# Performance work log

Hardware: AMD Instinct MI355X
Metric: run time of the kernel (lower is better)

The kernel has to match this reference:

```python
import jax, jax.numpy as jnp
import numpy as np

B, S, H, I, G = 2, 1024, 1024, 4096, 8


def setup_inputs() -> dict:
    key = jax.random.key(0)
    k1, k2, k3, k4 = jax.random.split(key, 4)
    # kaiming-style scaled init (scale matters only for numerics, not math)
    hidden_states = jax.random.normal(k1, (B, S, H), dtype=jnp.float32)
    WG = jax.random.normal(k2, (H, G), dtype=jnp.float32) * (1.0 / np.sqrt(H))
    Wi = jax.random.normal(k3, (G, H, I), dtype=jnp.float32) * (1.0 / np.sqrt(H))
    down = jax.random.normal(k4, (I, H), dtype=jnp.float32) * (1.0 / np.sqrt(I))
    return {"hidden_states": hidden_states, "WG": WG, "Wi": Wi, "down": down, "topk": 2}


def topk_sigmoid(gate, k):
    # gate: [B,S,G] -> sigmoid gated scores masked to top-k per token
    _, idx = jax.lax.top_k(gate, k)                       # idx: [B,S,k]
    mask = (idx[..., None] == jnp.arange(gate.shape[-1])).any(axis=-2)  # [B,S,G] bool
    return jax.nn.sigmoid(gate) * mask


def reference(hidden_states, WG, Wi, down, topk):
    gate = hidden_states @ WG                             # [B,S,G]
    g = topk_sigmoid(gate, topk)                          # [B,S,G]
    # dense contraction over all groups (faithful to original einsum)
    up = jnp.einsum('bse,bsg,geo->bso', hidden_states, g, Wi)  # [B,S,I]
    act = jnp.square(jax.nn.relu(up))                     # ReLU^2
    return act @ down                                     # [B,S,H]
```

## Files before the change

kernel.cpp:

```cpp
#include <hip/hip_runtime.h>
#include <hip/hip_bf16.h>

typedef unsigned short u16;
typedef short short8_t __attribute__((ext_vector_type(8)));
typedef float f32x4 __attribute__((ext_vector_type(4)));

#define GLOBAL_AS(p) ((const __attribute__((address_space(1))) void*)(p))
#define LDS_AS(p)    ((__attribute__((address_space(3))) void*)(p))

__device__ __forceinline__ u16 f2bf(float f) {
    union { float f; unsigned int u; } x;
    x.f = f;
    unsigned int r = x.u + 0x7fffu + ((x.u >> 16) & 1u);
    return (u16)(r >> 16);
}

#define M_NMT   0
#define M_TE    2
#define M_TB    42
#define M_PAIR  96
#define M_RTOK  4192
#define M_RW    9312

__global__ __launch_bounds__(64) void gate_topk_kernel(
    const float* __restrict__ h, const float* __restrict__ wg, float* __restrict__ w) {
    const int t = blockIdx.x;
    const int lane = threadIdx.x;
    float acc[8];
#pragma unroll
    for (int g = 0; g < 8; ++g) acc[g] = 0.f;
    for (int e = lane; e < 1024; e += 64) {
        float hv = h[(size_t)t * 1024 + e];
        float4 r0 = *(const float4*)&wg[e * 8];
        float4 r1 = *(const float4*)&wg[e * 8 + 4];
        acc[0] += hv * r0.x; acc[1] += hv * r0.y; acc[2] += hv * r0.z; acc[3] += hv * r0.w;
        acc[4] += hv * r1.x; acc[5] += hv * r1.y; acc[6] += hv * r1.z; acc[7] += hv * r1.w;
    }
#pragma unroll
    for (int off = 32; off > 0; off >>= 1) {
#pragma unroll
        for (int g = 0; g < 8; ++g) acc[g] += __shfl_down(acc[g], off);
    }
    if (lane == 0) {
        int i1 = 0;
        for (int g = 1; g < 8; ++g) if (acc[g] > acc[i1]) i1 = g;
        int i2 = -1;
        for (int g = 0; g < 8; ++g) {
            if (g == i1) continue;
            if (i2 < 0 || acc[g] > acc[i2]) i2 = g;
        }
#pragma unroll
        for (int g = 0; g < 8; ++g) {
            float v = (g == i1 || g == i2) ? (1.f / (1.f + __expf(-acc[g]))) : 0.f;
            w[t * 8 + g] = v;
        }
    }
}

__global__ __launch_bounds__(256) void scan_kernel(
    const float* __restrict__ w, int* __restrict__ meta) {
    __shared__ int cnt[8], pos[8];
    const int tid = threadIdx.x;
    if (tid < 8) cnt[tid] = 0;
    __syncthreads();
    for (int t = tid; t < 2048; t += 256) {
#pragma unroll
        for (int g = 0; g < 8; ++g)
            if (w[t * 8 + g] > 0.f) atomicAdd(&cnt[g], 1);
    }
    __syncthreads();
    if (tid == 0) {
        int base = 0, mt = 0;
        for (int e = 0; e < 8; ++e) {
            pos[e] = base;
            int nt = (cnt[e] + 127) >> 7;
            for (int k = 0; k < nt; ++k) { meta[M_TE + mt] = e; meta[M_TB + mt] = base + k * 128; ++mt; }
            base += nt << 7;
        }
        meta[M_NMT] = mt;
        meta[1] = base;
    }
    __syncthreads();
    for (int i = tid; i < 5120; i += 256) meta[M_RTOK + i] = -1;
    __syncthreads();
    float* row_w = (float*)&meta[M_RW];
    for (int t = tid; t < 2048; t += 256) {
        int slot = 0;
#pragma unroll
        for (int g = 0; g < 8; ++g) {
            float wv = w[t * 8 + g];
            if (wv > 0.f) {
                int p = atomicAdd(&pos[g], 1);
                meta[M_RTOK + p] = t;
                row_w[p] = wv;
                meta[M_PAIR + t * 2 + slot] = p;
                ++slot;
            }
        }
    }
}

__global__ __launch_bounds__(256) void gather_a_kernel(
    const float* __restrict__ h, const int* __restrict__ meta, u16* __restrict__ A) {
    const int row = blockIdx.x;
    const int tid = threadIdx.x;
    const int tok = meta[M_RTOK + row];
    u16* dst = A + (size_t)row * 1024;
    if (tok < 0) {
        uint2 z; z.x = 0u; z.y = 0u;
        ((uint2*)dst)[tid] = z;
        return;
    }
    const float wv = ((const float*)&meta[M_RW])[row];
    float4 v = ((const float4*)(h + (size_t)tok * 1024))[tid];
    u16 o[4] = { f2bf(v.x * wv), f2bf(v.y * wv), f2bf(v.z * wv), f2bf(v.w * wv) };
    ((uint2*)dst)[tid] = *(const uint2*)o;
}

__global__ __launch_bounds__(256, 2) void gemm1_sparse_kernel(
    const u16* __restrict__ A, const float* __restrict__ Wi,
    float* __restrict__ up, const int* __restrict__ meta) {
    const int mt = blockIdx.y;
    if (mt >= meta[M_NMT]) return;
    const int e = meta[M_TE + mt];
    const int base = meta[M_TB + mt];
    const int n0 = blockIdx.x * 128;
    const int K = 1024, N = 4096;
    const float* Bm = Wi + (size_t)e * K * N;

    __shared__ short a_tile[2][128 * 64];
    __shared__ short b_tile[2][128 * 64];
    const int tid = threadIdx.x;
    const int lane = tid & 63;
    const int wave = tid >> 6;
    const int wm = (wave >> 1) * 64;
    const int wn = (wave & 1) * 64;
    const int r = lane & 15;
    const int quad = lane >> 4;
    const int rowin = lane >> 3;
    const int achk = ((lane & 7) ^ (rowin & 7)) * 8;
    const int aldst = (lane & 7) * 8;
    const int bidx_n = tid & 127;
    const int bidx_k8 = tid >> 7;

    const f32x4 vzero = {0.f, 0.f, 0.f, 0.f};
    f32x4 acc[4][4];
#pragma unroll
    for (int i = 0; i < 4; ++i)
#pragma unroll
        for (int j = 0; j < 4; ++j) acc[i][j] = vzero;

    float bvA[4][8], bvB[4][8];

#define G1_LOADB(bv, kb_)                                                             \
    {                                                                                 \
        const int kbc = (kb_);                                                        \
        _Pragma("unroll")                                                             \
        for (int cb = 0; cb < 4; ++cb) {                                              \
            const float* bp = Bm + (size_t)(kbc + (bidx_k8 + cb * 2) * 8) * N + n0 + bidx_n; \
            _Pragma("unroll")                                                         \
            for (int kk = 0; kk < 8; ++kk) bv[cb][kk] = bp[(size_t)kk * N];            \
        }                                                                             \
    }

#define G1_STOREB(bv, buf)                                                            \
    {                                                                                 \
        _Pragma("unroll")                                                             \
        for (int cb = 0; cb < 4; ++cb) {                                              \
            int bk8 = bidx_k8 + cb * 2;                                               \
            u16 bc[8];                                                                \
            _Pragma("unroll")                                                         \
            for (int kk = 0; kk < 8; ++kk) bc[kk] = f2bf(bv[cb][kk]);                  \
            *(short8_t*)&b_tile[buf][bidx_n * 64 + ((bk8 ^ (bidx_n & 7)) * 8)] =       \
                *(const short8_t*)bc;                                                 \
        }                                                                             \
    }

#define G1_STAGEA(kb_, buf)                                                           \
    {                                                                                 \
        const int kbc = (kb_);                                                        \
        _Pragma("unroll")                                                             \
        for (int it = 0; it < 4; ++it) {                                              \
            int row = wave * 8 + it * 32 + rowin;                                     \
            const u16* ga = A + (size_t)(base + row) * K + kbc + achk;                \
            __builtin_amdgcn_global_load_lds(GLOBAL_AS(ga),                           \
                LDS_AS(&a_tile[buf][row * 64 + aldst]), 16, 0, 0);                    \
        }                                                                             \
    }

#define G1_COMPUTE(buf)                                                               \
    {                                                                                 \
        _Pragma("unroll")                                                             \
        for (int ks = 0; ks < 2; ++ks) {                                              \
            const int cp = ((ks * 4 + quad) ^ (r & 7)) * 8;                           \
            short8_t af[4], bfr[4];                                                   \
            _Pragma("unroll")                                                         \
            for (int i = 0; i < 4; ++i)                                               \
                af[i] = *(const short8_t*)&a_tile[buf][(wm + i * 16 + r) * 64 + cp];  \
            _Pragma("unroll")                                                         \
            for (int j = 0; j < 4; ++j)                                               \
                bfr[j] = *(const short8_t*)&b_tile[buf][(wn + j * 16 + r) * 64 + cp]; \
            _Pragma("unroll")                                                         \
            for (int i = 0; i < 4; ++i)                                               \
                _Pragma("unroll")                                                     \
                for (int j = 0; j < 4; ++j)                                           \
                    acc[i][j] = __builtin_amdgcn_mfma_f32_16x16x32_bf16(              \
                        af[i], bfr[j], acc[i][j], 0, 0, 0);                           \
        }                                                                             \
    }

    G1_LOADB(bvA, 0);
    G1_STAGEA(0, 0);
    G1_STOREB(bvA, 0);
    G1_LOADB(bvB, 64);
    __syncthreads();

    for (int t = 0; t < 14; t += 2) {
        G1_LOADB(bvA, (t + 2) * 64);
        __builtin_amdgcn_sched_barrier(0);
        G1_STAGEA((t + 1) * 64, 1);
        G1_STOREB(bvB, 1);
        G1_COMPUTE(0);
        __syncthreads();
        {
            int kbn = (t + 3) * 64; if (kbn > 960) kbn = 960;
            G1_LOADB(bvB, kbn);
        }
        __builtin_amdgcn_sched_barrier(0);
        G1_STAGEA((t + 2) * 64, 0);
        G1_STOREB(bvA, 0);
        G1_COMPUTE(1);
        __syncthreads();
    }
    G1_STAGEA(960, 1);
    G1_STOREB(bvB, 1);
    G1_COMPUTE(0);
    __syncthreads();
    G1_COMPUTE(1);

#undef G1_LOADB
#undef G1_STOREB
#undef G1_STAGEA
#undef G1_COMPUTE

#pragma unroll
    for (int i = 0; i < 4; ++i)
#pragma unroll
        for (int j = 0; j < 4; ++j)
#pragma unroll
            for (int reg = 0; reg < 4; ++reg) {
                int cr = base + wm + i * 16 + quad * 4 + reg;
                int cc = n0 + wn + j * 16 + r;
                up[(size_t)cr * N + cc] = acc[i][j][reg];
            }
}

__global__ __launch_bounds__(256) void combine_kernel(
    const float* __restrict__ up, const int* __restrict__ meta, u16* __restrict__ act) {
    const int t = blockIdx.x;
    const int tid = threadIdx.x;
    const int p0 = meta[M_PAIR + t * 2];
    const int p1 = meta[M_PAIR + t * 2 + 1];
    const float* r0 = up + (size_t)p0 * 4096;
    const float* r1 = up + (size_t)p1 * 4096;
    u16* dst = act + (size_t)t * 4096;
#pragma unroll
    for (int it = 0; it < 4; ++it) {
        int i = (tid + it * 256) * 4;
        float4 a = *(const float4*)&r0[i];
        float4 b = *(const float4*)&r1[i];
        float s0 = a.x + b.x, s1 = a.y + b.y, s2 = a.z + b.z, s3 = a.w + b.w;
        s0 = s0 > 0.f ? s0 * s0 : 0.f;
        s1 = s1 > 0.f ? s1 * s1 : 0.f;
        s2 = s2 > 0.f ? s2 * s2 : 0.f;
        s3 = s3 > 0.f ? s3 * s3 : 0.f;
        u16 o[4] = { f2bf(s0), f2bf(s1), f2bf(s2), f2bf(s3) };
        *(uint2*)&dst[i] = *(const uint2*)o;
    }
}

__global__ __launch_bounds__(256) void transpose_cvt_kernel(
    const float* __restrict__ in, u16* __restrict__ out, int R, int C) {
    __shared__ u16 tile[64][65];
    const int rt = blockIdx.y * 64;
    const int ct = blockIdx.x * 64;
    const int tid = threadIdx.x;
#pragma unroll
    for (int it = 0; it < 2; ++it) {
        int r = (tid >> 3) + it * 32;
        int c8 = (tid & 7) * 8;
        const float* ip = &in[(size_t)(rt + r) * C + ct + c8];
        float4 v0 = *(const float4*)ip;
        float4 v1 = *(const float4*)(ip + 4);
        tile[c8 + 0][r] = f2bf(v0.x); tile[c8 + 1][r] = f2bf(v0.y);
        tile[c8 + 2][r] = f2bf(v0.z); tile[c8 + 3][r] = f2bf(v0.w);
        tile[c8 + 4][r] = f2bf(v1.x); tile[c8 + 5][r] = f2bf(v1.y);
        tile[c8 + 6][r] = f2bf(v1.z); tile[c8 + 7][r] = f2bf(v1.w);
    }
    __syncthreads();
#pragma unroll
    for (int it = 0; it < 2; ++it) {
        int c = (tid >> 3) + it * 32;
        int r8 = (tid & 7) * 8;
        u16 tmp[8];
#pragma unroll
        for (int j = 0; j < 8; ++j) tmp[j] = tile[c][r8 + j];
        *(uint4*)&out[(size_t)(ct + c) * R + rt + r8] = *(const uint4*)tmp;
    }
}

template <int BM, int WROWS, int WCOLS>
__global__ __launch_bounds__(256) void gemm_tn_kernel(
    const u16* __restrict__ X, const u16* __restrict__ Y, float* __restrict__ Cout,
    int M, int N, int K) {
    constexpr int WM = BM / WROWS;
    constexpr int WN = 128 / WCOLS;
    constexpr int FI = WM / 16;
    constexpr int FJ = WN / 16;
    __shared__ short a_tile[2][BM * 64];
    __shared__ short b_tile[2][128 * 64];
    const int tid = threadIdx.x;
    const int lane = tid & 63;
    const int wave = tid >> 6;

    const int Nt = gridDim.x, Mt = gridDim.y;
    const int lid = blockIdx.y * Nt + blockIdx.x;
    const int xcd = lid & 7;
    const int p = lid >> 3;
    const int n_tile = xcd * (Nt >> 3) + p / Mt;
    const int m_tile = p % Mt;
    const int m0 = m_tile * BM;
    const int n0 = n_tile * 128;

    const int wm = (wave / WCOLS) * WM;
    const int wn = (wave % WCOLS) * WN;
    const int rowin = lane >> 3;
    const int achk = ((lane & 7) ^ (rowin & 7)) * 8;
    const int aldst = (lane & 7) * 8;
    const int r = lane & 15;
    const int quad = lane >> 4;

    const f32x4 vzero = {0.f, 0.f, 0.f, 0.f};
    f32x4 acc[FI][FJ];
#pragma unroll
    for (int i = 0; i < FI; ++i)
#pragma unroll
        for (int j = 0; j < FJ; ++j) acc[i][j] = vzero;

#define G2_STAGE(kb_, buf)                                                            \
    {                                                                                 \
        const int kbc = (kb_);                                                        \
        _Pragma("unroll")                                                             \
        for (int it = 0; it < BM / 32; ++it) {                                        \
            int row = wave * 8 + it * 32 + rowin;                                     \
            const u16* ga = X + (size_t)(m0 + row) * K + kbc + achk;                  \
            __builtin_amdgcn_global_load_lds(GLOBAL_AS(ga),                           \
                LDS_AS(&a_tile[buf][row * 64 + aldst]), 16, 0, 0);                    \
        }                                                                             \
        _Pragma("unroll")                                                             \
        for (int it = 0; it < 4; ++it) {                                              \
            int row = wave * 8 + it * 32 + rowin;                                     \
            const u16* gb = Y + (size_t)(n0 + row) * K + kbc + achk;                  \
            __builtin_amdgcn_global_load_lds(GLOBAL_AS(gb),                           \
                LDS_AS(&b_tile[buf][row * 64 + aldst]), 16, 0, 0);                    \
        }                                                                             \
    }

#define G2_COMPUTE(buf)                                                               \
    {                                                                                 \
        _Pragma("unroll")                                                             \
        for (int ks = 0; ks < 2; ++ks) {                                              \
            const int cp = ((ks * 4 + quad) ^ (r & 7)) * 8;                           \
            short8_t af[FI], bfr[FJ];                                                 \
            _Pragma("unroll")                                                         \
            for (int i = 0; i < FI; ++i)                                              \
                af[i] = *(const short8_t*)&a_tile[buf][(wm + i * 16 + r) * 64 + cp];  \
            _Pragma("unroll")                                                         \
            for (int j = 0; j < FJ; ++j)                                              \
                bfr[j] = *(const short8_t*)&b_tile[buf][(wn + j * 16 + r) * 64 + cp]; \
            _Pragma("unroll")                                                         \
            for (int i = 0; i < FI; ++i)                                              \
                _Pragma("unroll")                                                     \
                for (int j = 0; j < FJ; ++j)                                          \
                    acc[i][j] = __builtin_amdgcn_mfma_f32_16x16x32_bf16(              \
                        af[i], bfr[j], acc[i][j], 0, 0, 0);                           \
        }                                                                             \
    }

    const int nk = K >> 6;
    G2_STAGE(0, 0);
    __syncthreads();
    for (int t = 0; t < nk - 1; ++t) {
        const int nxt = (t + 1) & 1;
        G2_STAGE((t + 1) * 64, nxt);
        G2_COMPUTE(t & 1);
        __syncthreads();
    }
    G2_COMPUTE((nk - 1) & 1);

#undef G2_STAGE
#undef G2_COMPUTE

#pragma unroll
    for (int i = 0; i < FI; ++i)
#pragma unroll
        for (int j = 0; j < FJ; ++j)
#pragma unroll
            for (int reg = 0; reg < 4; ++reg) {
                int cr = m0 + wm + i * 16 + quad * 4 + reg;
                int cc = n0 + wn + j * 16 + r;
                Cout[(size_t)cr * N + cc] = acc[i][j][reg];
            }
}

extern "C" void kernel_launch(void* const* d_in, const int* in_sizes, int n_in,
                              void* d_out, int out_size, void* d_ws, size_t ws_size,
                              hipStream_t stream) {
    const float* h    = (const float*)d_in[0];
    const float* WG   = (const float*)d_in[1];
    const float* Wi   = (const float*)d_in[2];
    const float* down = (const float*)d_in[3];
    float* out = (float*)d_out;

    const int T = 2048, H = 1024, I = 4096;

    char* ws = (char*)d_ws;
    float* w_gate = (float*)(ws);
    int*   meta   = (int*)(ws + 65536);
    u16*   Arow   = (u16*)(ws + 131072);
    float* up     = (float*)(ws + 131072 + 10485760);
    u16*   act    = (u16*)(ws + 131072 + 10485760 + 83886080);
    u16*   downT  = (u16*)(ws + 131072 + 10485760 + 83886080 + 16777216);

    gate_topk_kernel<<<T, 64, 0, stream>>>(h, WG, w_gate);
    scan_kernel<<<1, 256, 0, stream>>>(w_gate, meta);
    gather_a_kernel<<<5120, 256, 0, stream>>>(h, meta, Arow);

    gemm1_sparse_kernel<<<dim3(32, 40), 256, 0, stream>>>(Arow, Wi, up, meta);

    combine_kernel<<<T, 256, 0, stream>>>(up, meta, act);

    transpose_cvt_kernel<<<dim3(H / 64, I / 64), 256, 0, stream>>>(down, downT, I, H);
    gemm_tn_kernel<64, 1, 4><<<dim3(H / 128, T / 64), 256, 0, stream>>>(
        act, downT, out, T, H, I);
}
```

Measured before the change: 393.4 us.

## Restructure gemm1 B pipeline to single LDS buffer with asm loads; retile gemm2

```diff
diff --git a/kernel.cpp b/kernel.cpp
--- a/kernel.cpp
+++ b/kernel.cpp
@@ -57,13 +57,13 @@
     }
 }
 
-__global__ __launch_bounds__(256) void scan_kernel(
+__global__ __launch_bounds__(1024) void scan_kernel(
     const float* __restrict__ w, int* __restrict__ meta) {
     __shared__ int cnt[8], pos[8];
     const int tid = threadIdx.x;
     if (tid < 8) cnt[tid] = 0;
     __syncthreads();
-    for (int t = tid; t < 2048; t += 256) {
+    for (int t = tid; t < 2048; t += 1024) {
 #pragma unroll
         for (int g = 0; g < 8; ++g)
             if (w[t * 8 + g] > 0.f) atomicAdd(&cnt[g], 1);
@@ -81,10 +81,10 @@
         meta[1] = base;
     }
     __syncthreads();
-    for (int i = tid; i < 5120; i += 256) meta[M_RTOK + i] = -1;
+    for (int i = tid; i < 5120; i += 1024) meta[M_RTOK + i] = -1;
     __syncthreads();
     float* row_w = (float*)&meta[M_RW];
-    for (int t = tid; t < 2048; t += 256) {
+    for (int t = tid; t < 2048; t += 1024) {
         int slot = 0;
 #pragma unroll
         for (int g = 0; g < 8; ++g) {
@@ -117,7 +117,7 @@
     ((uint2*)dst)[tid] = *(const uint2*)o;
 }
 
-__global__ __launch_bounds__(256, 2) void gemm1_sparse_kernel(
+__global__ __launch_bounds__(256) void gemm1_sparse_kernel(
     const u16* __restrict__ A, const float* __restrict__ Wi,
     float* __restrict__ up, const int* __restrict__ meta) {
     const int mt = blockIdx.y;
@@ -129,7 +129,7 @@
     const float* Bm = Wi + (size_t)e * K * N;
 
     __shared__ short a_tile[2][128 * 64];
-    __shared__ short b_tile[2][128 * 64];
+    __shared__ short b_tile[128 * 64];
     const int tid = threadIdx.x;
     const int lane = tid & 63;
     const int wave = tid >> 6;
@@ -140,6 +140,7 @@
     const int rowin = lane >> 3;
     const int achk = ((lane & 7) ^ (rowin & 7)) * 8;
     const int aldst = (lane & 7) * 8;
+
     const int bidx_n = tid & 127;
     const int bidx_k8 = tid >> 7;
 
@@ -150,9 +151,9 @@
 #pragma unroll
         for (int j = 0; j < 4; ++j) acc[i][j] = vzero;
 
-    float bvA[4][8], bvB[4][8];
-
-#define G1_LOADB(bv, kb_)                                                             \
+    float bv[4][8];
+
+#define G1_LOADB_C(kb_)                                                               \
     {                                                                                 \
         const int kbc = (kb_);                                                        \
         _Pragma("unroll")                                                             \
@@ -163,7 +164,21 @@
         }                                                                             \
     }
 
-#define G1_STOREB(bv, buf)                                                            \
+#define G1_LOADB_ASM(kb_)                                                             \
+    {                                                                                 \
+        const int kbc = (kb_);                                                        \
+        _Pragma("unroll")                                                             \
+        for (int cb = 0; cb < 4; ++cb) {                                              \
+            const float* bp = Bm + (size_t)(kbc + (bidx_k8 + cb * 2) * 8) * N + n0 + bidx_n; \
+            _Pragma("unroll")                                                         \
+            for (int kk = 0; kk < 8; ++kk) {                                          \
+                asm volatile("global_load_dword %0, %1, off"                          \
+                             : "=v"(bv[cb][kk]) : "v"(bp + (size_t)kk * N));          \
+            }                                                                         \
+        }                                                                             \
+    }
+
+#define G1_STOREB()                                                                   \
     {                                                                                 \
         _Pragma("unroll")                                                             \
         for (int cb = 0; cb < 4; ++cb) {                                              \
@@ -171,7 +186,7 @@
             u16 bc[8];                                                                \
             _Pragma("unroll")                                                         \
             for (int kk = 0; kk < 8; ++kk) bc[kk] = f2bf(bv[cb][kk]);                  \
-            *(short8_t*)&b_tile[buf][bidx_n * 64 + ((bk8 ^ (bidx_n & 7)) * 8)] =       \
+            *(short8_t*)&b_tile[bidx_n * 64 + ((bk8 ^ (bidx_n & 7)) * 8)] =            \
                 *(const short8_t*)bc;                                                 \
         }                                                                             \
     }
@@ -199,7 +214,7 @@
                 af[i] = *(const short8_t*)&a_tile[buf][(wm + i * 16 + r) * 64 + cp];  \
             _Pragma("unroll")                                                         \
             for (int j = 0; j < 4; ++j)                                               \
-                bfr[j] = *(const short8_t*)&b_tile[buf][(wn + j * 16 + r) * 64 + cp]; \
+                bfr[j] = *(const short8_t*)&b_tile[(wn + j * 16 + r) * 64 + cp];      \
             _Pragma("unroll")                                                         \
             for (int i = 0; i < 4; ++i)                                               \
                 _Pragma("unroll")                                                     \
@@ -209,36 +224,27 @@
         }                                                                             \
     }
 
-    G1_LOADB(bvA, 0);
+    G1_LOADB_C(0);
     G1_STAGEA(0, 0);
-    G1_STOREB(bvA, 0);
-    G1_LOADB(bvB, 64);
-    __syncthreads();
-
-    for (int t = 0; t < 14; t += 2) {
-        G1_LOADB(bvA, (t + 2) * 64);
+    G1_STOREB();
+    __syncthreads();
+
+    for (int kb = 0; kb < 16; ++kb) {
+        if (kb < 15) {
+            G1_LOADB_ASM((kb + 1) * 64);
+            G1_STAGEA((kb + 1) * 64, (kb + 1) & 1);
+        }
+        G1_COMPUTE(kb & 1);
+        __syncthreads();
         __builtin_amdgcn_sched_barrier(0);
-        G1_STAGEA((t + 1) * 64, 1);
-        G1_STOREB(bvB, 1);
-        G1_COMPUTE(0);
-        __syncthreads();
-        {
-            int kbn = (t + 3) * 64; if (kbn > 960) kbn = 960;
-            G1_LOADB(bvB, kbn);
-        }
-        __builtin_amdgcn_sched_barrier(0);
-        G1_STAGEA((t + 2) * 64, 0);
-        G1_STOREB(bvA, 0);
-        G1_COMPUTE(1);
-        __syncthreads();
-    }
-    G1_STAGEA(960, 1);
-    G1_STOREB(bvB, 1);
-    G1_COMPUTE(0);
-    __syncthreads();
-    G1_COMPUTE(1);
-
-#undef G1_LOADB
+        if (kb < 15) {
+            G1_STOREB();
+            __syncthreads();
+        }
+    }
+
+#undef G1_LOADB_C
+#undef G1_LOADB_ASM
 #undef G1_STOREB
 #undef G1_STAGEA
 #undef G1_COMPUTE
@@ -433,7 +439,7 @@
     u16*   downT  = (u16*)(ws + 131072 + 10485760 + 83886080 + 16777216);
 
     gate_topk_kernel<<<T, 64, 0, stream>>>(h, WG, w_gate);
-    scan_kernel<<<1, 256, 0, stream>>>(w_gate, meta);
+    scan_kernel<<<1, 1024, 0, stream>>>(w_gate, meta);
     gather_a_kernel<<<5120, 256, 0, stream>>>(h, meta, Arow);
 
     gemm1_sparse_kernel<<<dim3(32, 40), 256, 0, stream>>>(Arow, Wi, up, meta);
@@ -441,6 +447,6 @@
     combine_kernel<<<T, 256, 0, stream>>>(up, meta, act);
 
     transpose_cvt_kernel<<<dim3(H / 64, I / 64), 256, 0, stream>>>(down, downT, I, H);
-    gemm_tn_kernel<64, 1, 4><<<dim3(H / 128, T / 64), 256, 0, stream>>>(
+    gemm_tn_kernel<32, 1, 4><<<dim3(H / 128, T / 32), 256, 0, stream>>>(
         act, downT, out, T, H, I);
 }
```

Result: faster. 366.1 us (-6.9%).
